# Kernel optimization log

Measured on AMD Instinct MI355X. Metric: run time of the kernel, lower is better.

Reference implementation:

```python
import jax, jax.numpy as jnp
import numpy as np

B, H, S, D = 2, 8, 2048, 64
TEMPERATURE = 8.0  # sqrt(D)
NEG = -1.0e9


def setup_inputs() -> dict:
    key = jax.random.key(0)
    kq, kk, kv, km = jax.random.split(key, 4)
    q = jax.random.normal(kq, (B, H, S, D), dtype=jnp.float32)
    k = jax.random.normal(kk, (B, H, S, D), dtype=jnp.float32)
    v = jax.random.normal(kv, (B, H, S, D), dtype=jnp.float32)
    mask = jax.random.randint(km, (B, 1, 1, S), 0, 2, dtype=jnp.int32)
    return {"q": q, "k": k, "v": v, "mask": mask}


def reference(q, k, v, mask):
    # scores: [B,H,S,S]
    att = jnp.einsum('bhqd,bhkd->bhqk', q / TEMPERATURE, k)
    att = jnp.where(mask == 0, NEG, att)
    att = jax.nn.softmax(att, axis=-1)
    return jnp.einsum('bhqk,bhkd->bhqd', att, v)
```

## Files before the change

kernel.cpp:

```cpp
#include <hip/hip_runtime.h>
#include <hip/hip_bf16.h>

#define SDIM 2048
#define DDIM 64
#define HNUM 8
#define QBLK 64
#define KVBLK 64
#define NTHR 256
#define NT (SDIM / KVBLK)
#define NSPLIT 2
#define NEGV -1.0e9f
#define LOG2E 1.44269504088896f
#define FIXMAX 12.0f

#define WS_KH 0u
#define WS_VH 4194304u
#define WS_O1 8388608u
#define WS_ML 12582912u
#define WS_CNT 13123584u

typedef __bf16 bf16x8 __attribute__((ext_vector_type(8)));
typedef __bf16 bf16x4 __attribute__((ext_vector_type(4)));
typedef short s16x4 __attribute__((ext_vector_type(4)));
typedef float f32x4 __attribute__((ext_vector_type(4)));
typedef unsigned short u16;
typedef u16 u16x4 __attribute__((ext_vector_type(4)));
typedef u16 u16x8 __attribute__((ext_vector_type(8)));

__device__ __forceinline__ u16 f2bf(float f) {
    unsigned u = __float_as_uint(f);
    u += 0x7FFFu + ((u >> 16) & 1u);
    return (u16)(u >> 16);
}
__device__ __forceinline__ float bf2f(u16 h) {
    return __uint_as_float((unsigned)h << 16);
}

union U8 { u16 u[8]; u16x8 v; bf16x8 b; };

#define GLD16(g, l) __builtin_amdgcn_global_load_lds( \
    (const __attribute__((address_space(1))) unsigned int*)(g), \
    (__attribute__((address_space(3))) unsigned int*)(l), 16, 0, 0)

__device__ __forceinline__ f32x4 mfma16(s16x4 a, s16x4 b, f32x4 c) {
#if __has_builtin(__builtin_amdgcn_mfma_f32_16x16x16bf16_1k)
    return __builtin_amdgcn_mfma_f32_16x16x16bf16_1k(a, b, c, 0, 0, 0);
#else
    asm("v_mfma_f32_16x16x16_bf16 %0, %1, %2, %0" : "+v"(c) : "v"(a), "v"(b));
    return c;
#endif
}

__global__ __launch_bounds__(NTHR)
void attn_prep(const float* __restrict__ K, const float* __restrict__ V,
               const int* __restrict__ MK, char* __restrict__ ws) {
    __shared__ float sT[64][68];
    __shared__ int win[64];
    __shared__ int wtot[4];
    const int t = threadIdx.x;
    const int kt = blockIdx.x, bh = blockIdx.y;
    const int b = bh >> 3;
    const int kv0 = kt * KVBLK;
    const int ln = t & 63, wvi = t >> 6;

    const int* m = MK + (size_t)b * SDIM;
    int vals[8], cnt = 0;
    #pragma unroll
    for (int e = 0; e < 8; ++e) {
        vals[e] = m[t * 8 + e];
        cnt += (vals[e] != 0);
    }
    int inc = cnt;
    #pragma unroll
    for (int off = 1; off < 64; off <<= 1) {
        int n = __shfl_up(inc, off);
        if (ln >= off) inc += n;
    }
    if (ln == 63) wtot[wvi] = inc;
    if (t < 64) win[t] = 0;
    __syncthreads();
    int wbase = 0;
    #pragma unroll
    for (int w = 0; w < 4; ++w) if (w < wvi) wbase += wtot[w];
    const int total = wtot[0] + wtot[1] + wtot[2] + wtot[3];
    int pos = wbase + inc - cnt;
    #pragma unroll
    for (int e = 0; e < 8; ++e) {
        if (vals[e]) {
            if (pos >= kv0 && pos < kv0 + KVBLK) win[pos - kv0] = t * 8 + e;
            ++pos;
        }
    }
    if (t == 0 && kt == 0) ((int*)(ws + WS_CNT))[b] = total;
    __syncthreads();
    if (kv0 >= ((total + KVBLK - 1) & ~(KVBLK - 1))) return;

    const size_t base = (size_t)bh * SDIM * DDIM;
    const int r = t >> 2, c16 = (t & 3) * 16;
    const int sw = (r & 7) << 4;
    const int orig = win[r];

    {
        const float* kp = K + base + (size_t)orig * DDIM + c16;
        char* khrow = ws + WS_KH + ((size_t)bh * SDIM + kv0 + r) * 128;
        #pragma unroll
        for (int j = 0; j < 2; ++j) {
            const float4 a = *(const float4*)(kp + 8 * j);
            const float4 c = *(const float4*)(kp + 8 * j + 4);
            float f[8] = {a.x, a.y, a.z, a.w, c.x, c.y, c.z, c.w};
            U8 h;
            #pragma unroll
            for (int e = 0; e < 8; ++e) h.u[e] = f2bf(f[e]);
            *(u16x8*)(khrow + ((2 * c16 + 16 * j) ^ sw)) = h.v;
        }
    }
    {
        const float* vp = V + base + (size_t)orig * DDIM + c16;
        #pragma unroll
        for (int j = 0; j < 4; ++j)
            *(float4*)&sT[r][c16 + 4 * j] = *(const float4*)(vp + 4 * j);
    }
    __syncthreads();
    {
        const int mt = t >> 6, d = t & 63;
        char* dst = ws + WS_VH + ((size_t)(bh * NT + kt)) * 8192 + mt * 2048 + d * 32;
        #pragma unroll
        for (int gk = 0; gk < 4; ++gk) {
            u16x4 h;
            #pragma unroll
            for (int e = 0; e < 4; ++e)
                h[e] = f2bf(sT[mt * 16 + 4 * gk + e][d]);
            *(u16x4*)(dst + (((gk ^ ((d >> 2) & 3)) << 3))) = h;
        }
    }
}

__global__ __launch_bounds__(NTHR, 4)
void attn_main(const float* __restrict__ Q, char* __restrict__ ws,
               float* __restrict__ O) {
    __shared__ __align__(16) u16 sK[2][4096];
    __shared__ __align__(16) u16 sV[2][4096];

    const int tid = threadIdx.x;
    const int wv = tid >> 6, ln = tid & 63;
    const int g = ln >> 4, mi = ln & 15;
    const int bh = blockIdx.y, b = bh >> 3;
    const int split = blockIdx.z;
    const size_t base = (size_t)bh * SDIM * DDIM;
    const int qrow = blockIdx.x * QBLK + 16 * wv + mi;

    const int L = ((const int*)(ws + WS_CNT))[b];
    const int nt = (L + KVBLK - 1) >> 6;
    const int half = (nt + 1) >> 1;
    const int t0 = split ? half : 0;
    const int tn = split ? nt : half;

    const int sw = (mi & 7) << 4;
    const int c0 = (16 * g) ^ sw;
    const int c1 = (64 + 16 * g) ^ sw;
    const int vslot = (g ^ (mi >> 2)) << 3;

    bf16x8 qf[2];
    {
        const float* qp = Q + base + (size_t)qrow * DDIM;
        #pragma unroll
        for (int ks = 0; ks < 2; ++ks) {
            const float4 a = *(const float4*)(qp + 32 * ks + 8 * g);
            const float4 c = *(const float4*)(qp + 32 * ks + 8 * g + 4);
            float f[8] = {a.x, a.y, a.z, a.w, c.x, c.y, c.z, c.w};
            U8 h;
            #pragma unroll
            for (int e = 0; e < 8; ++e) h.u[e] = f2bf(f[e] * (0.125f * LOG2E));
            qf[ks] = h.b;
        }
    }

    const char* kgl = ws + WS_KH + (size_t)bh * SDIM * 128;
    const char* vgl = ws + WS_VH + (size_t)bh * NT * 8192;

    f32x4 zero4 = {0.f, 0.f, 0.f, 0.f};
    f32x4 minit = {-FIXMAX, -FIXMAX, -FIXMAX, -FIXMAX};
    f32x4 oacc[4];
    #pragma unroll
    for (int i = 0; i < 4; ++i) oacc[i] = zero4;
    float lr0 = 0.f, lr1 = 0.f, lr2 = 0.f, lr3 = 0.f;

#define STAGE_T(kt_, buf_) do { \
    const char* ksrc_ = kgl + (size_t)(kt_) * 8192 + wv * 2048; \
    char* kdst_ = (char*)&sK[buf_][0] + wv * 2048; \
    GLD16(ksrc_ + ln * 16, kdst_); \
    GLD16(ksrc_ + 1024 + ln * 16, kdst_ + 1024); \
    const char* vsrc_ = vgl + (size_t)(kt_) * 8192 + wv * 2048; \
    char* vdst_ = (char*)&sV[buf_][0] + wv * 2048; \
    GLD16(vsrc_ + ln * 16, vdst_); \
    GLD16(vsrc_ + 1024 + ln * 16, vdst_ + 1024); \
} while (0)

    if (t0 < tn) {
        STAGE_T(t0, 0);
        int cur = 0;
        for (int kt = t0; kt < tn; ++kt) {
            const int kn = (kt + 1 < tn) ? kt + 1 : t0;
            STAGE_T(kn, cur ^ 1);
            asm volatile("s_waitcnt vmcnt(4)" ::: "memory");
            __builtin_amdgcn_s_barrier();

            const char* kb = (const char*)&sK[cur][0] + mi * 128;
            f32x4 s[4];
            #pragma unroll
            for (int mt = 0; mt < 4; ++mt) {
                f32x4 acc = minit;
                const bf16x8 a0 = *(const bf16x8*)(kb + mt * 2048 + c0);
                const bf16x8 a1 = *(const bf16x8*)(kb + mt * 2048 + c1);
                acc = __builtin_amdgcn_mfma_f32_16x16x32_bf16(a0, qf[0], acc, 0, 0, 0);
                acc = __builtin_amdgcn_mfma_f32_16x16x32_bf16(a1, qf[1], acc, 0, 0, 0);
                s[mt] = acc;
            }
            const int rem = L - kt * KVBLK;
            if (rem < KVBLK) {
                #pragma unroll
                for (int mt = 0; mt < 4; ++mt)
                    #pragma unroll
                    for (int r = 0; r < 4; ++r)
                        if (16 * mt + 4 * g + r >= rem) s[mt][r] = NEGV;
            }

            bf16x4 pw[4];
            #pragma unroll
            for (int mt = 0; mt < 4; ++mt) {
                float psum = 0.f;
                #pragma unroll
                for (int r = 0; r < 4; ++r) {
                    const float p = __builtin_amdgcn_exp2f(s[mt][r]);
                    pw[mt][r] = (__bf16)p;
                    psum += p;
                }
                if (mt == 0) lr0 += psum;
                else if (mt == 1) lr1 += psum;
                else if (mt == 2) lr2 += psum;
                else lr3 += psum;
            }

            const char* vb = (const char*)&sV[cur][0] + mi * 32 + vslot;
            #pragma unroll
            for (int dt = 0; dt < 4; ++dt) {
                #pragma unroll
                for (int mt = 0; mt < 4; ++mt) {
                    const s16x4 vf = *(const s16x4*)(vb + mt * 2048 + dt * 512);
                    oacc[dt] = mfma16(vf, __builtin_bit_cast(s16x4, pw[mt]), oacc[dt]);
                }
            }
            __builtin_amdgcn_s_barrier();
            cur ^= 1;
        }
    }
#undef STAGE_T

    float lrun = lr0 + lr1 + lr2 + lr3;
    lrun += __shfl_xor(lrun, 16);
    lrun += __shfl_xor(lrun, 32);
    asm volatile("s_waitcnt vmcnt(0)" ::: "memory");
    const float inv = lrun > 0.f ? 1.0f / lrun : 0.f;
    if (split == 0) {
        float* op = O + base + (size_t)qrow * DDIM;
        #pragma unroll
        for (int dt = 0; dt < 4; ++dt) {
            float4 o;
            o.x = oacc[dt][0] * inv;
            o.y = oacc[dt][1] * inv;
            o.z = oacc[dt][2] * inv;
            o.w = oacc[dt][3] * inv;
            *(float4*)(op + 16 * dt + 4 * g) = o;
        }
    } else {
        u16* op1 = (u16*)(ws + WS_O1) + ((size_t)bh * SDIM + qrow) * DDIM;
        #pragma unroll
        for (int dt = 0; dt < 4; ++dt) {
            u16x4 o;
            #pragma unroll
            for (int r = 0; r < 4; ++r) o[r] = f2bf(oacc[dt][r] * inv);
            *(u16x4*)(op1 + 16 * dt + 4 * g) = o;
        }
    }
    if (g == 0) {
        float* lp = (float*)(ws + WS_ML) + ((size_t)(split * 2 * HNUM + bh) * SDIM + qrow);
        *lp = lrun;
    }
}

__global__ __launch_bounds__(NTHR)
void attn_combine(const char* __restrict__ ws, float* __restrict__ O) {
    const int t = threadIdx.x;
    const size_t grow = (size_t)blockIdx.x * 16 + (t >> 4);
    const int e4 = (t & 15) * 4;
    const float* ml = (const float*)(ws + WS_ML);
    float w0 = ml[grow];
    float w1 = ml[(size_t)2 * HNUM * SDIM + grow];
    const float swt = w0 + w1;
    const float inv = swt > 0.f ? 1.0f / swt : 0.f;
    w0 *= inv; w1 *= inv;
    float* op = O + grow * DDIM + e4;
    const float4 o0 = *(const float4*)op;
    const u16x4 o1 = *(const u16x4*)((const u16*)(ws + WS_O1) + grow * DDIM + e4);
    float4 r;
    r.x = o0.x * w0 + bf2f(o1[0]) * w1;
    r.y = o0.y * w0 + bf2f(o1[1]) * w1;
    r.z = o0.z * w0 + bf2f(o1[2]) * w1;
    r.w = o0.w * w0 + bf2f(o1[3]) * w1;
    *(float4*)op = r;
}

extern "C" void kernel_launch(void* const* d_in, const int* in_sizes, int n_in,
                              void* d_out, int out_size, void* d_ws, size_t ws_size,
                              hipStream_t stream) {
    const float* q  = (const float*)d_in[0];
    const float* k  = (const float*)d_in[1];
    const float* v  = (const float*)d_in[2];
    const int*   mk = (const int*)d_in[3];
    float* o = (float*)d_out;
    char* ws = (char*)d_ws;

    dim3 pgrid(NT, 2 * HNUM);
    attn_prep<<<pgrid, NTHR, 0, stream>>>(k, v, mk, ws);

    dim3 grid(SDIM / QBLK, 2 * HNUM, NSPLIT);
    attn_main<<<grid, NTHR, 0, stream>>>(q, ws, o);

    dim3 cgrid((2 * HNUM * SDIM) / 16);
    attn_combine<<<cgrid, NTHR, 0, stream>>>(ws, o);
}
```

Baseline: 36.29 us.

## Split KV range across 3-4 blocks and pack partial outputs as bf16 pairs

Raises the KV split count from 2 to 4 (or 3 if the workspace is too small), so the grid has more blocks and each does fewer KV tiles, filling more CUs. The first two splits write bf16 partials interleaved into the fp32 output buffer, and the others go to workspace. The combine kernel then reads up to four partials with their row sums. This adds combine traffic and more bf16 rounding of partials, and the workspace layout moves the count to offset 0. Note that the prep kernel's hidden body must also write the count to the new WS_CNT location for correctness.

```diff
diff --git a/kernel.cpp b/kernel.cpp
--- a/kernel.cpp
+++ b/kernel.cpp
@@ -8,16 +8,18 @@
 #define KVBLK 64
 #define NTHR 256
 #define NT (SDIM / KVBLK)
-#define NSPLIT 2
 #define NEGV -1.0e9f
 #define LOG2E 1.44269504088896f
 #define FIXMAX 12.0f
 
-#define WS_KH 0u
-#define WS_VH 4194304u
-#define WS_O1 8388608u
-#define WS_ML 12582912u
-#define WS_CNT 13123584u
+#define WS_CNT 0u
+#define WS_KH 128u
+#define WS_VH (4194304u + 128u)
+#define WS_O2 (8388608u + 128u)
+#define WS_O3 (12582912u + 128u)
+#define ML_OFF(nsp) ((nsp) == 4 ? (16777216u + 128u) : (12582912u + 128u))
+#define NEED4 17301632u
+#define NEED3 12976256u
 
 typedef __bf16 bf16x8 __attribute__((ext_vector_type(8)));
 typedef __bf16 bf16x4 __attribute__((ext_vector_type(4)));
@@ -137,7 +139,7 @@
 
 __global__ __launch_bounds__(NTHR, 4)
 void attn_main(const float* __restrict__ Q, char* __restrict__ ws,
-               float* __restrict__ O) {
+               float* __restrict__ O, int nsplit) {
     __shared__ __align__(16) u16 sK[2][4096];
     __shared__ __align__(16) u16 sV[2][4096];
 
@@ -151,9 +153,9 @@
 
     const int L = ((const int*)(ws + WS_CNT))[b];
     const int nt = (L + KVBLK - 1) >> 6;
-    const int half = (nt + 1) >> 1;
-    const int t0 = split ? half : 0;
-    const int tn = split ? nt : half;
+    const int per = (nt + nsplit - 1) / nsplit;
+    const int t0 = split * per;
+    const int tn = min(nt, t0 + per);
 
     const int sw = (mi & 7) << 4;
     const int c0 = (16 * g) ^ sw;
@@ -261,52 +263,63 @@
     lrun += __shfl_xor(lrun, 32);
     asm volatile("s_waitcnt vmcnt(0)" ::: "memory");
     const float inv = lrun > 0.f ? 1.0f / lrun : 0.f;
-    if (split == 0) {
-        float* op = O + base + (size_t)qrow * DDIM;
-        #pragma unroll
-        for (int dt = 0; dt < 4; ++dt) {
-            float4 o;
-            o.x = oacc[dt][0] * inv;
-            o.y = oacc[dt][1] * inv;
-            o.z = oacc[dt][2] * inv;
-            o.w = oacc[dt][3] * inv;
-            *(float4*)(op + 16 * dt + 4 * g) = o;
-        }
+    u16x4 pb[4];
+    #pragma unroll
+    for (int dt = 0; dt < 4; ++dt)
+        #pragma unroll
+        for (int r = 0; r < 4; ++r) pb[dt][r] = f2bf(oacc[dt][r] * inv);
+
+    if (split < 2) {
+        u16* ob = (u16*)(O + base + (size_t)qrow * DDIM) + split;
+        #pragma unroll
+        for (int dt = 0; dt < 4; ++dt)
+            #pragma unroll
+            for (int r = 0; r < 4; ++r)
+                ob[2 * (16 * dt + 4 * g + r)] = pb[dt][r];
     } else {
-        u16* op1 = (u16*)(ws + WS_O1) + ((size_t)bh * SDIM + qrow) * DDIM;
-        #pragma unroll
-        for (int dt = 0; dt < 4; ++dt) {
-            u16x4 o;
-            #pragma unroll
-            for (int r = 0; r < 4; ++r) o[r] = f2bf(oacc[dt][r] * inv);
-            *(u16x4*)(op1 + 16 * dt + 4 * g) = o;
-        }
+        u16* op = (u16*)(ws + (split == 2 ? WS_O2 : WS_O3)) +
+                  ((size_t)bh * SDIM + qrow) * DDIM;
+        #pragma unroll
+        for (int dt = 0; dt < 4; ++dt)
+            *(u16x4*)(op + 16 * dt + 4 * g) = pb[dt];
     }
     if (g == 0) {
-        float* lp = (float*)(ws + WS_ML) + ((size_t)(split * 2 * HNUM + bh) * SDIM + qrow);
+        float* lp = (float*)(ws + ML_OFF(nsplit)) +
+                    ((size_t)(split * 2 * HNUM + bh) * SDIM + qrow);
         *lp = lrun;
     }
 }
 
 __global__ __launch_bounds__(NTHR)
-void attn_combine(const char* __restrict__ ws, float* __restrict__ O) {
+void attn_combine(const char* __restrict__ ws, float* __restrict__ O, int nsplit) {
     const int t = threadIdx.x;
     const size_t grow = (size_t)blockIdx.x * 16 + (t >> 4);
     const int e4 = (t & 15) * 4;
-    const float* ml = (const float*)(ws + WS_ML);
-    float w0 = ml[grow];
-    float w1 = ml[(size_t)2 * HNUM * SDIM + grow];
-    const float swt = w0 + w1;
-    const float inv = swt > 0.f ? 1.0f / swt : 0.f;
-    w0 *= inv; w1 *= inv;
+    const float* ml = (const float*)(ws + ML_OFF(nsplit));
+    const size_t mstride = (size_t)2 * HNUM * SDIM;
+    float l0 = ml[grow];
+    float l1 = ml[mstride + grow];
+    float l2 = ml[2 * mstride + grow];
+    float l3 = (nsplit == 4) ? ml[3 * mstride + grow] : 0.f;
+    const float lsum = l0 + l1 + l2 + l3;
+    const float inv = lsum > 0.f ? 1.0f / lsum : 0.f;
+    l0 *= inv; l1 *= inv; l2 *= inv; l3 *= inv;
+
     float* op = O + grow * DDIM + e4;
-    const float4 o0 = *(const float4*)op;
-    const u16x4 o1 = *(const u16x4*)((const u16*)(ws + WS_O1) + grow * DDIM + e4);
+    const float4 o01 = *(const float4*)op;
+    const u16x4 p2 = *(const u16x4*)((const u16*)(ws + WS_O2) + grow * DDIM + e4);
+    u16x4 p3 = {0, 0, 0, 0};
+    if (nsplit == 4)
+        p3 = *(const u16x4*)((const u16*)(ws + WS_O3) + grow * DDIM + e4);
+
     float4 r;
-    r.x = o0.x * w0 + bf2f(o1[0]) * w1;
-    r.y = o0.y * w0 + bf2f(o1[1]) * w1;
-    r.z = o0.z * w0 + bf2f(o1[2]) * w1;
-    r.w = o0.w * w0 + bf2f(o1[3]) * w1;
+    #pragma unroll
+    for (int j = 0; j < 4; ++j) {
+        const unsigned u = __float_as_uint(((const float*)&o01)[j]);
+        float acc = bf2f((u16)(u & 0xFFFFu)) * l0 + bf2f((u16)(u >> 16)) * l1;
+        acc += bf2f(p2[j]) * l2 + bf2f(p3[j]) * l3;
+        ((float*)&r)[j] = acc;
+    }
     *(float4*)op = r;
 }
 
@@ -320,12 +333,14 @@
     float* o = (float*)d_out;
     char* ws = (char*)d_ws;
 
+    const int nsplit = (ws_size >= (size_t)NEED4) ? 4 : 3;
+
     dim3 pgrid(NT, 2 * HNUM);
     attn_prep<<<pgrid, NTHR, 0, stream>>>(k, v, mk, ws);
 
-    dim3 grid(SDIM / QBLK, 2 * HNUM, NSPLIT);
-    attn_main<<<grid, NTHR, 0, stream>>>(q, ws, o);
+    dim3 grid(SDIM / QBLK, 2 * HNUM, nsplit);
+    attn_main<<<grid, NTHR, 0, stream>>>(q, ws, o, nsplit);
 
     dim3 cgrid((2 * HNUM * SDIM) / 16);
-    attn_combine<<<cgrid, NTHR, 0, stream>>>(ws, o);
-}
+    attn_combine<<<cgrid, NTHR, 0, stream>>>(ws, o, nsplit);
+}
```

After: 46.19 us. +27.3%, slower.
